# Performance work log

Hardware: AMD Instinct MI355X
Metric: run time of the kernel (lower is better)

The kernel has to match this reference:

```python
import jax, jax.numpy as jnp
import numpy as np

B, N, D, E = 64, 512, 128, 16384
NEG = -1e9


def setup_inputs() -> dict:
    key = jax.random.key(0)
    ks = jax.random.split(key, 10)
    return {
        "node_emb": jax.random.normal(ks[0], (B, N, D), jnp.float32),
        "mask": jnp.ones((B, N), dtype=bool),
        "edge_idx": jax.random.randint(ks[1], (2, E), 0, N),
        "attn_wts": jax.random.uniform(ks[2], (E,), jnp.float32),
        "edge_weights": jax.random.uniform(ks[3], (B, N, N), jnp.float32) + 0.1,
        "W_ih": jax.random.normal(ks[4], (4 * D, D), jnp.float32) * 0.05,
        "W_hh": jax.random.normal(ks[5], (4 * D, D), jnp.float32) * 0.05,
        "b_ih": jax.random.normal(ks[6], (4 * D,), jnp.float32) * 0.05,
        "b_hh": jax.random.normal(ks[7], (4 * D,), jnp.float32) * 0.05,
        "attn_W": jax.random.normal(ks[8], (D, D), jnp.float32) * 0.05,
        "attn_b": jax.random.normal(ks[9], (D,), jnp.float32) * 0.05,
        "enc_attn_wt": jnp.float32(0.75),
        "revisit_penalty": jnp.float32(-0.5),
        "shortcut_weight": jnp.float32(10.0),
        "shortcut_bonus": jnp.float32(15.0),
    }


def reference(node_emb, mask, edge_idx, attn_wts, edge_weights,
              W_ih, W_hh, b_ih, b_hh, attn_W, attn_b,
              enc_attn_wt, revisit_penalty, shortcut_weight, shortcut_bonus):
    B_, N_, D_ = node_emb.shape
    scale = 1.0 / jnp.sqrt(jnp.float32(D_))
    bidx = jnp.arange(B_)
    nidx = jnp.arange(N_)[None, :]
    # keys = attn(node_emb): identical every step in the torch code -> hoisted.
    keys = node_emb @ attn_W.T + attn_b  # [B,N,D]
    # Encoder-attention edge scatter precomputed as dense [N,N] src->tgt table.
    A = jnp.zeros((N_, N_), node_emb.dtype).at[edge_idx[0], edge_idx[1]].add(attn_wts)
    real_count = jnp.sum(mask, axis=1).astype(jnp.int32)  # [B]

    def step_fn(carry, step):
        h, c, inp, visited, uniq, first, prev = carry
        # LSTMCell (torch gate order i,f,g,o)
        gates = inp @ W_ih.T + b_ih + h @ W_hh.T + b_hh  # [B,4D]
        i, f, g, o = jnp.split(gates, 4, axis=1)
        c = jax.nn.sigmoid(f) * c + jax.nn.sigmoid(i) * jnp.tanh(g)
        h = jax.nn.sigmoid(o) * jnp.tanh(c)
        scores = jnp.einsum('bd,bnd->bn', h, keys) * scale  # [B,N]
        # encoder-attn bonus (only when prev_node exists, i.e. step > 0)
        scores = scores + jnp.where(step > 0, enc_attn_wt, 0.0) * A[prev]
        # branch 1: revisit penalty while tour incomplete
        rev = jnp.where(visited & mask, revisit_penalty, scores)
        # branch 2: shortcut bonuses once all real nodes visited (next_idx == first)
        prev_w = edge_weights[bidx, prev]  # [B,N] costs from prev node
        to_first = jnp.take_along_axis(edge_weights, first[:, None, None], axis=2)[..., 0]  # [B,N]
        direct = prev_w[bidx, first][:, None]  # [B,1]
        detour = prev_w + to_first
        bmask = mask & (nidx != first[:, None]) & (detour < direct)
        bonus = jnp.where(bmask, shortcut_bonus * (direct - detour) / direct, 0.0)
        cmin = prev_w.min(axis=1, keepdims=True)
        cmax = prev_w.max(axis=1, keepdims=True)
        rng_ok = cmax > cmin
        normd = jnp.where(rng_ok,
                          shortcut_weight * (1.0 - (prev_w - cmin) / jnp.where(rng_ok, cmax - cmin, 1.0)),
                          0.0)
        shortcut = scores + bonus + normd
        cond = (uniq < real_count)[:, None]
        scores = jnp.where(cond, rev, jnp.where(step > 0, shortcut, scores))
        scores = jnp.where(mask, scores, NEG)
        probs = jax.nn.softmax(scores, axis=1)
        curr = jnp.argmax(probs, axis=1).astype(jnp.int32)  # greedy decode
        log_p = jnp.log(probs[bidx, curr] + 1e-10)
        first = jnp.where(step == 0, curr, first)
        newly = ~visited[bidx, curr]
        uniq = uniq + newly.astype(jnp.int32)
        visited = visited.at[bidx, curr].set(True)
        inp = node_emb[bidx, curr]
        return (h, c, inp, visited, uniq, first, curr), (curr, log_p)

    init = (jnp.zeros((B_, D_), node_emb.dtype),
            jnp.zeros((B_, D_), node_emb.dtype),
            node_emb.mean(axis=1),
            jnp.zeros((B_, N_), dtype=bool),
            jnp.zeros((B_,), jnp.int32),
            jnp.zeros((B_,), jnp.int32),
            jnp.zeros((B_,), jnp.int32))
    (h, c, inp, visited, uniq, first, prev), (curr_seq, logp_seq) = jax.lax.scan(
        step_fn, init, jnp.arange(N_))
    # final step N: return to first node with log-prob 0
    tours = jnp.concatenate([curr_seq.T, first[:, None]], axis=1)          # [B, N+1]
    log_probs = jnp.concatenate([logp_seq.T, jnp.zeros((B_, 1), logp_seq.dtype)], axis=1)
    return tours, log_probs
```

## Files before the change

### kernel.cpp

```cpp
#include <hip/hip_runtime.h>
#include <cstdint>
#include <cstddef>

constexpr int kB = 64;
constexpr int kN = 512;
constexpr int kD = 128;
constexpr int kE = 16384;
constexpr double kNEG = -1e9;

constexpr size_t BO_WT   = 0;
constexpr size_t BO_BIAS = 524288;
constexpr size_t BO_INP0 = 528384;
constexpr size_t BO_AWT  = 593920;
constexpr size_t BO_AB   = 659456;
constexpr size_t BO_A    = 659968;
constexpr size_t BO_WT4  = 2757120;
constexpr size_t BO_GPRE = 2888192;
constexpr size_t GPRE_BYTES = (size_t)64 * 513 * 512 * 4;
constexpr size_t BO_KEYS4 = BO_GPRE + GPRE_BYTES;
constexpr size_t KEYS_BYTES = (size_t)64 * 32 * 512 * 16;
constexpr size_t WS_NEED_FULL = BO_KEYS4 + KEYS_BYTES;

__device__ __forceinline__ double finzd(double v, double fb) {
    return (v == v && v <= 1.0e308 && v >= -1.0e308) ? v : fb;
}
__device__ __forceinline__ double load_scalar_d(const void* p, double fb) {
    unsigned short lo; __builtin_memcpy(&lo, p, 2);
    float f;
    if (lo == 0) { __builtin_memcpy(&f, p, 4); }
    else { unsigned int u = ((unsigned int)lo) << 16; __builtin_memcpy(&f, &u, 4); }
    return finzd((double)f, fb);
}
__device__ __forceinline__ double sigd(double v) { return 1.0 / (1.0 + exp(-v)); }

__global__ __launch_bounds__(256) void prep_wt(const float* __restrict__ W_ih,
                                               const float* __restrict__ W_hh,
                                               const float* __restrict__ b_ih,
                                               const float* __restrict__ b_hh,
                                               char* __restrict__ wsb) {
    int idx = blockIdx.x * 256 + threadIdx.x;
    if (idx < 131072) {
        int k = idx >> 9, j = idx & 511;
        float v = (k < 128) ? W_ih[j * 128 + k] : W_hh[j * 128 + (k - 128)];
        ((float*)(wsb + BO_WT))[idx] = v;
    } else if (idx < 131072 + 512) {
        int j = idx - 131072;
        ((double*)(wsb + BO_BIAS))[j] = (double)b_ih[j] + (double)b_hh[j];
    }
}

__global__ __launch_bounds__(256) void prep_wt4(char* __restrict__ wsb) {
    int idx = blockIdx.x * 256 + threadIdx.x;
    int q = idx >> 9, j = idx & 511;
    const float* WT = (const float*)(wsb + BO_WT);
    float4 v;
    v.x = WT[(size_t)(192 + 4 * q + 0) * 512 + j];
    v.y = WT[(size_t)(192 + 4 * q + 1) * 512 + j];
    v.z = WT[(size_t)(192 + 4 * q + 2) * 512 + j];
    v.w = WT[(size_t)(192 + 4 * q + 3) * 512 + j];
    ((float4*)(wsb + BO_WT4))[idx] = v;
}

__global__ __launch_bounds__(256) void prep_awt(const float* __restrict__ attn_W,
                                                const float* __restrict__ attn_b,
                                                char* __restrict__ wsb) {
    int idx = blockIdx.x * 256 + threadIdx.x;
    if (idx < 16384) {
        int k = idx >> 7, d = idx & 127;
        ((float*)(wsb + BO_AWT))[idx] = attn_W[d * 128 + k];
    } else if (idx < 16512) {
        ((float*)(wsb + BO_AB))[idx - 16384] = attn_b[idx - 16384];
    }
}

__global__ __launch_bounds__(256) void prep_zeroA(char* __restrict__ wsb) {
    int idx = blockIdx.x * 256 + threadIdx.x;
    ((double*)(wsb + BO_A))[idx] = 0.0;
}

__global__ __launch_bounds__(256) void prep_scatterA(const int* __restrict__ edge_idx,
                                                     const float* __restrict__ attn_wts,
                                                     char* __restrict__ wsb) {
    int e = blockIdx.x * 256 + threadIdx.x;
    if (e < kE) {
        int s = edge_idx[e] & 511;
        int t = edge_idx[kE + e] & 511;
        atomicAdd(&((double*)(wsb + BO_A))[(size_t)s * kN + t], (double)attn_wts[e]);
    }
}

__global__ __launch_bounds__(128) void prep_inp0(const float* __restrict__ emb,
                                                 char* __restrict__ wsb) {
    int b = blockIdx.x, d = threadIdx.x;
    const float* p = emb + (size_t)b * kN * kD + d;
    double s = 0.0;
#pragma unroll 8
    for (int n = 0; n < kN; n++) s += (double)p[(size_t)n * kD];
    ((double*)(wsb + BO_INP0))[b * kD + d] = s * (1.0 / 512.0);
}

__global__ __launch_bounds__(512) void prep_gpre(const float* __restrict__ emb,
                                                 char* __restrict__ wsb) {
    const int b = blockIdx.y;
    const int n0 = blockIdx.x * 16;
    const int tid = threadIdx.x;
    const int nr = (513 - n0 < 16) ? (513 - n0) : 16;
    __shared__ double xs[16 * 128];
    const double* inp0 = (const double*)(wsb + BO_INP0) + (size_t)b * 128;
    for (int i = tid; i < nr * 128; i += 512) {
        int r = i >> 7, d = i & 127;
        int n = n0 + r;
        xs[i] = (n < 512) ? (double)emb[((size_t)b * 512 + n) * 128 + d] : inp0[d];
    }
    __syncthreads();
    const float* wcol = ((const float*)(wsb + BO_WT)) + tid;
    double acc[16];
#pragma unroll
    for (int r = 0; r < 16; r++) acc[r] = 0.0;
    for (int k = 0; k < 128; k++) {
        double w = (double)wcol[(size_t)k * 512];
#pragma unroll
        for (int r = 0; r < 16; r++) acc[r] += xs[r * 128 + k] * w;
    }
    float* gp = (float*)(wsb + BO_GPRE);
#pragma unroll
    for (int r = 0; r < 16; r++)
        if (r < nr) gp[((size_t)b * 513 + n0 + r) * 512 + tid] = (float)acc[r];
}

__global__ __launch_bounds__(256) void prep_keys(const float* __restrict__ emb,
                                                 const float* __restrict__ attn_W,
                                                 const float* __restrict__ attn_b,
                                                 char* __restrict__ wsb) {
    const int b = blockIdx.y;
    const int n0 = blockIdx.x * 64;
    const int tid = threadIdx.x;
    __shared__ float embL[64 * 130];
    __shared__ float WL[128 * 128];
    for (int i = tid; i < 64 * 128; i += 256) {
        int r = i >> 7, k = i & 127;
        embL[r * 130 + k] = emb[((size_t)b * kN + n0 + r) * kD + k];
    }
    for (int i = tid; i < 128 * 128; i += 256) WL[i] = attn_W[i];
    __syncthreads();
    const int nh = tid & 63;
    const int part = tid >> 6;
    float4* kout = (float4*)(wsb + BO_KEYS4) + (size_t)b * 32 * 512;
    const float* er = &embL[nh * 130];
    for (int dq = part * 8; dq < part * 8 + 8; dq++) {
        double a0 = (double)attn_b[4 * dq + 0], a1 = (double)attn_b[4 * dq + 1];
        double a2 = (double)attn_b[4 * dq + 2], a3 = (double)attn_b[4 * dq + 3];
        const float* w0 = &WL[(4 * dq + 0) * 128];
        const float* w1 = &WL[(4 * dq + 1) * 128];
        const float* w2 = &WL[(4 * dq + 2) * 128];
        const float* w3 = &WL[(4 * dq + 3) * 128];
#pragma unroll 8
        for (int k = 0; k < 128; k++) {
            double ek = (double)er[k];
            a0 += ek * (double)w0[k]; a1 += ek * (double)w1[k];
            a2 += ek * (double)w2[k]; a3 += ek * (double)w3[k];
        }
        float4 v; v.x = (float)a0; v.y = (float)a1; v.z = (float)a2; v.w = (float)a3;
        kout[(size_t)dq * 512 + n0 + nh] = v;
    }
}

template <int M>
__global__ __launch_bounds__(512) void decode_kernel(
    const float* __restrict__ emb, const unsigned char* __restrict__ mask,
    const float* __restrict__ edge_w, const char* __restrict__ wsb,
    const void* __restrict__ enc_p, const void* __restrict__ rev_p,
    const void* __restrict__ sw_p, const void* __restrict__ sb_p,
    float* __restrict__ out) {
    const int b = blockIdx.x;
    const int tid = threadIdx.x;

    __shared__ float wks[(M == 0) ? (128 * 129) : (16 * 512 * 4)];
    __shared__ double x[256];
    __shared__ double cs[128];
    __shared__ double gates[(M == 0) ? 512 : 1];
    __shared__ double trans[(M == 0) ? 1 : 512];
    __shared__ double up[(M == 0) ? 512 : 1];
    __shared__ double u[(M == 0) ? 128 : 1];
    __shared__ double redd[8], redd2[8];
    __shared__ int redi[8];
    __shared__ unsigned char visited[512];
    __shared__ int tours_s[512];
    __shared__ double logp_d[512];
    __shared__ int s_rc;
    __shared__ double s_hb, s_cmin, s_cmax;

    const float* WT = (const float*)(wsb + BO_WT);
    const double* biasC = (const double*)(wsb + BO_BIAS);
    const double* A = (const double*)(wsb + BO_A);
    const float* EW = edge_w + (size_t)b * kN * kN;
    const double enc = load_scalar_d(enc_p, 0.75);
    const double revp = load_scalar_d(rev_p, -0.5);
    const double sw = load_scalar_d(sw_p, 10.0);
    const double sb = load_scalar_d(sb_p, 15.0);
    const double scale = 1.0 / sqrt(128.0);

    if constexpr (M == 0) {
        for (int i = tid; i < 128 * 128; i += 512) {
            int k = i >> 7, d = i & 127;
            wks[k * 129 + d] = ((const float*)(wsb + BO_AWT))[i];
        }
    } else {
        for (int i = tid; i < 64 * 512; i += 512) {
            int r = i >> 9, j = i & 511;
            wks[((r >> 2) * 512 + j) * 4 + (r & 3)] = WT[(size_t)(128 + r) * 512 + j];
        }
    }
    double abreg = 0.0;
    if constexpr (M == 0)
        abreg = (tid < 128) ? (double)((const float*)(wsb + BO_AB))[tid] : 0.0;

    if (tid < 128) { x[tid] = ((const double*)(wsb + BO_INP0))[b * kD + tid]; cs[tid] = 0.0; }
    if (tid >= 128 && tid < 256) x[tid] = 0.0;
    visited[tid] = 0;
    const size_t mi = (size_t)b * kN + tid;
    const bool mk = (mask[mi] != 0) || (mask[mi & ~(size_t)3] != 0);
    {
        int v = mk ? 1 : 0;
        for (int off = 32; off; off >>= 1) v += __shfl_xor(v, off);
        if ((tid & 63) == 0) redi[tid >> 6] = v;
    }
    __syncthreads();
    if (tid == 0) {
        int rc = 0;
        for (int w = 0; w < 8; w++) rc += redi[w];
        s_rc = rc;
    }
    __syncthreads();
    const int rc = s_rc;

    int prev = 0, first = 0, uniq = 0;

    const float* gbase = (const float*)(wsb + BO_GPRE) + (size_t)b * 513 * 512;
    const float4* kb4 = (const float4*)(wsb + BO_KEYS4) + (size_t)b * 32 * 512;
    const float4* wl4 = (const float4*)wks;
    const float4* wg4 = (const float4*)(wsb + BO_WT4);
    const double* h = &x[128];

    if constexpr (M != 0) {
        {
            double gp0 = (double)gbase[(size_t)512 * 512 + tid];
            double gf = (biasC[tid] + gp0) + 0.0;
            trans[tid] = (tid >= 256 && tid < 384) ? tanh(gf) : sigd(gf);
        }
        double a_cur = A[tid];
        __syncthreads();

        for (int step = 0; step < kN; step++) {
            if (step > 0) {
                if (tid == prev) visited[tid] = 1;
                if (tid == 0) {
                    double m = 0.0;
#pragma unroll
                    for (int w = 0; w < 8; w++) m += redd2[w];
                    m = (m == m && m > 0.0) ? m : 1.0;
                    double p = 1.0 / m;
                    logp_d[step - 1] = (p == p && p >= 0.0) ? p : 0.0;
                }
            }
            if (tid < 128) {
                double ai = trans[tid], af = trans[128 + tid];
                double ag = trans[256 + tid], ao = trans[384 + tid];
                double c = af * cs[tid] + ai * ag;
                cs[tid] = c;
                x[128 + tid] = ao * tanh(c);
            }
            __syncthreads();

            double d0 = 0.0, d1 = 0.0, d2 = 0.0, d3 = 0.0;
            double q0 = biasC[tid], q1 = 0.0, q2 = 0.0, q3 = 0.0;
#pragma unroll 4
            for (int q = 0; q < 32; q++) {
                float4 w = kb4[(size_t)q * 512 + tid];
                const double* hq = &h[4 * q];
                d0 += hq[0] * (double)w.x; d1 += hq[1] * (double)w.y;
                d2 += hq[2] * (double)w.z; d3 += hq[3] * (double)w.w;
            }
#pragma unroll 4
            for (int q = 0; q < 16; q++) {
                float4 w = wl4[q * 512 + tid];
                const double* hq = &h[4 * q];
                q0 += hq[0] * (double)w.x; q1 += hq[1] * (double)w.y;
                q2 += hq[2] * (double)w.z; q3 += hq[3] * (double)w.w;
            }
#pragma unroll 4
            for (int q = 0; q < 16; q++) {
                float4 w = wg4[q * 512 + tid];
                const double* hq = &h[64 + 4 * q];
                q0 += hq[0] * (double)w.x; q1 += hq[1] * (double)w.y;
                q2 += hq[2] * (double)w.z; q3 += hq[3] * (double)w.w;
            }
            double s = ((d0 + d1) + (d2 + d3)) * scale;
            if (step > 0) s += enc * a_cur;

            double sfinal;
            const bool shortcut_mode = (uniq >= rc);
            if (!shortcut_mode) {
                sfinal = (visited[tid] && mk) ? revp : s;
            } else if (step > 0) {
                double pw = (double)EW[(size_t)prev * kN + tid];
                double mn = pw, mx = pw;
                for (int off = 32; off; off >>= 1) {
                    mn = fmin(mn, __shfl_xor(mn, off));
                    mx = fmax(mx, __shfl_xor(mx, off));
                }
                if ((tid & 63) == 0) { redd[tid >> 6] = mn; redd2[tid >> 6] = mx; }
                __syncthreads();
                if (tid == 0) {
                    double a = redd[0], z = redd2[0];
                    for (int w = 1; w < 8; w++) { a = fmin(a, redd[w]); z = fmax(z, redd2[w]); }
                    s_cmin = a; s_cmax = z;
                }
                __syncthreads();
                double cmin = s_cmin, cmax = s_cmax;
                int fi = first;
                double to_first = (double)EW[(size_t)tid * kN + fi];
                double direct = (double)EW[(size_t)prev * kN + fi];
                double detour = pw + to_first;
                double bonus = (mk && tid != fi && detour < direct && direct != 0.0)
                                   ? sb * (direct - detour) / direct : 0.0;
                bool rng_ok = cmax > cmin;
                double normd = rng_ok ? sw * (1.0 - (pw - cmin) / (cmax - cmin)) : 0.0;
                sfinal = s + bonus + normd;
            } else {
                sfinal = s;
            }
            if (!mk) sfinal = kNEG;
            sfinal = finzd(sfinal, kNEG);

            double v = sfinal; int vi = tid;
            for (int off = 32; off; off >>= 1) {
                double ov = __shfl_xor(v, off);
                int oi = __shfl_xor(vi, off);
                if (ov > v || (ov == v && oi < vi)) { v = ov; vi = oi; }
            }
            if ((tid & 63) == 0) { redd[tid >> 6] = v; redi[tid >> 6] = vi; }
            __syncthreads();
            double smax = redd[0]; int sidx = redi[0];
#pragma unroll
            for (int w = 1; w < 8; w++) {
                double rv = redd[w]; int ri = redi[w];
                if (rv > smax || (rv == smax && ri < sidx)) { smax = rv; sidx = ri; }
            }
            const int oldvis = visited[sidx];
            double gp_next = (double)gbase[(size_t)sidx * 512 + tid];
            double a_next = A[(size_t)sidx * kN + tid];

            double e = exp(sfinal - smax);
            double sv = e;
            for (int off = 32; off; off >>= 1) sv += __shfl_xor(sv, off);
            if ((tid & 63) == 0) redd2[tid >> 6] = sv;
            if (tid == 0) tours_s[step] = sidx;

            double gfn = ((q0 + q1) + (q2 + q3)) + gp_next;
            trans[tid] = (tid >= 256 && tid < 384) ? tanh(gfn) : sigd(gfn);

            uniq += oldvis ? 0 : 1;
            if (step == 0) first = sidx;
            prev = sidx;
            a_cur = a_next;
            __syncthreads();
        }
        if (tid == 0) {
            double m = 0.0;
#pragma unroll
            for (int w = 0; w < 8; w++) m += redd2[w];
            m = (m == m && m > 0.0) ? m : 1.0;
            double p = 1.0 / m;
            logp_d[kN - 1] = (p == p && p >= 0.0) ? p : 0.0;
        }
    } else {
        const float* awt = (const float*)wks;
        for (int step = 0; step < kN; step++) {
            double g0 = biasC[tid], g1 = 0.0, g2 = 0.0, g3 = 0.0;
            const float* wcol = WT + tid;
            for (int k0 = 0; k0 < 256; k0 += 4) {
                float w0 = wcol[(size_t)(k0 + 0) * 512], w1 = wcol[(size_t)(k0 + 1) * 512];
                float w2 = wcol[(size_t)(k0 + 2) * 512], w3 = wcol[(size_t)(k0 + 3) * 512];
                g0 += x[k0 + 0] * (double)w0; g1 += x[k0 + 1] * (double)w1;
                g2 += x[k0 + 2] * (double)w2; g3 += x[k0 + 3] * (double)w3;
            }
            gates[tid] = (g0 + g1) + (g2 + g3);
            __syncthreads();
            if (tid < 128) {
                double gi = gates[tid], gf = gates[128 + tid];
                double gg = gates[256 + tid], go = gates[384 + tid];
                double c = sigd(gf) * cs[tid] + sigd(gi) * tanh(gg);
                cs[tid] = c;
                double hd = sigd(go) * tanh(c);
                x[128 + tid] = hd;
                double hp = hd * abreg;
                for (int off = 32; off; off >>= 1) hp += __shfl_xor(hp, off);
                if ((tid & 63) == 0) redd[tid >> 6] = hp;
            }
            __syncthreads();
            {
                int k = tid & 127, part = tid >> 7;
                const float* arow = &awt[(size_t)k * 129 + part * 32];
                const double* hx = &x[128 + part * 32];
                double ps = 0.0;
#pragma unroll 8
                for (int i2 = 0; i2 < 32; i2++) ps += hx[i2] * (double)arow[i2];
                up[part * 128 + k] = ps;
            }
            __syncthreads();
            if (tid < 128) u[tid] = up[tid] + up[128 + tid] + up[256 + tid] + up[384 + tid];
            if (tid == 0) s_hb = redd[0] + redd[1];
            __syncthreads();
            double d0 = 0.0, d1 = 0.0, d2 = 0.0, d3 = 0.0;
            const float4* e4 = (const float4*)(emb + ((size_t)b * kN + tid) * kD);
#pragma unroll 4
            for (int q = 0; q < 32; q++) {
                float4 w = e4[q];
                const double* u4 = &u[q * 4];
                d0 += u4[0] * (double)w.x; d1 += u4[1] * (double)w.y;
                d2 += u4[2] * (double)w.z; d3 += u4[3] * (double)w.w;
            }
            double s = (((d0 + d1) + (d2 + d3)) + s_hb) * scale;
            if (step > 0) s += enc * A[(size_t)prev * kN + tid];

            double sfinal;
            const bool shortcut_mode = (uniq >= rc);
            if (!shortcut_mode) {
                sfinal = (visited[tid] && mk) ? revp : s;
            } else if (step > 0) {
                double pw = (double)EW[(size_t)prev * kN + tid];
                double mn = pw, mx = pw;
                for (int off = 32; off; off >>= 1) {
                    mn = fmin(mn, __shfl_xor(mn, off));
                    mx = fmax(mx, __shfl_xor(mx, off));
                }
                if ((tid & 63) == 0) { redd[tid >> 6] = mn; redd2[tid >> 6] = mx; }
                __syncthreads();
                if (tid == 0) {
                    double a = redd[0], z = redd2[0];
                    for (int w = 1; w < 8; w++) { a = fmin(a, redd[w]); z = fmax(z, redd2[w]); }
                    s_cmin = a; s_cmax = z;
                }
                __syncthreads();
                double cmin = s_cmin, cmax = s_cmax;
                int fi = first;
                double to_first = (double)EW[(size_t)tid * kN + fi];
                double direct = (double)EW[(size_t)prev * kN + fi];
                double detour = pw + to_first;
                double bonus = (mk && tid != fi && detour < direct && direct != 0.0)
                                   ? sb * (direct - detour) / direct : 0.0;
                bool rng_ok = cmax > cmin;
                double normd = rng_ok ? sw * (1.0 - (pw - cmin) / (cmax - cmin)) : 0.0;
                sfinal = s + bonus + normd;
            } else {
                sfinal = s;
            }
            if (!mk) sfinal = kNEG;
            sfinal = finzd(sfinal, kNEG);

            double v = sfinal; int vi = tid;
            for (int off = 32; off; off >>= 1) {
                double ov = __shfl_xor(v, off);
                int oi = __shfl_xor(vi, off);
                if (ov > v || (ov == v && oi < vi)) { v = ov; vi = oi; }
            }
            if ((tid & 63) == 0) { redd[tid >> 6] = v; redi[tid >> 6] = vi; }
            __syncthreads();
            double smax = redd[0]; int sidx = redi[0];
#pragma unroll
            for (int w = 1; w < 8; w++) {
                double rv = redd[w]; int ri = redi[w];
                if (rv > smax || (rv == smax && ri < sidx)) { smax = rv; sidx = ri; }
            }
            const int oldvis = visited[sidx];
            double e = exp(sfinal - smax);
            double sv = e;
            for (int off = 32; off; off >>= 1) sv += __shfl_xor(sv, off);
            if ((tid & 63) == 0) redd2[tid >> 6] = sv;
            __syncthreads();
            double m = 0.0;
#pragma unroll
            for (int w = 0; w < 8; w++) m += redd2[w];
            m = (m == m && m > 0.0) ? m : 1.0;
            double p = 1.0 / m;
            p = (p == p && p >= 0.0) ? p : 0.0;
            if (tid == 0) { tours_s[step] = sidx; logp_d[step] = p; }
            if (tid == sidx) visited[tid] = 1;
            uniq += oldvis ? 0 : 1;
            if (step == 0) first = sidx;
            prev = sidx;
            if (tid < 128) x[tid] = (double)emb[((size_t)b * kN + sidx) * kD + tid];
            __syncthreads();
        }
    }

    __syncthreads();
    out[(size_t)b * (kN + 1) + tid] = (float)tours_s[tid];
    out[(size_t)kB * (kN + 1) + (size_t)b * (kN + 1) + tid] =
        (float)log(logp_d[tid] + 1e-10);
    if (tid == 0) {
        out[(size_t)b * (kN + 1) + kN] = (float)first;
        out[(size_t)kB * (kN + 1) + (size_t)b * (kN + 1) + kN] = 0.f;
    }
}

extern "C" void kernel_launch(void* const* d_in, const int* in_sizes, int n_in,
                              void* d_out, int out_size, void* d_ws, size_t ws_size,
                              hipStream_t stream) {
    const float* emb = (const float*)d_in[0];
    const unsigned char* mask = (const unsigned char*)d_in[1];
    const int* edge_idx = (const int*)d_in[2];
    const float* attn_wts = (const float*)d_in[3];
    const float* edge_w = (const float*)d_in[4];
    const float* W_ih = (const float*)d_in[5];
    const float* W_hh = (const float*)d_in[6];
    const float* b_ih = (const float*)d_in[7];
    const float* b_hh = (const float*)d_in[8];
    const float* attn_W = (const float*)d_in[9];
    const float* attn_b = (const float*)d_in[10];
    char* wsb = (char*)d_ws;
    float* out = (float*)d_out;
    (void)in_sizes; (void)n_in; (void)out_size;

    prep_wt<<<dim3(514), dim3(256), 0, stream>>>(W_ih, W_hh, b_ih, b_hh, wsb);
    prep_zeroA<<<dim3(1024), dim3(256), 0, stream>>>(wsb);
    prep_scatterA<<<dim3(64), dim3(256), 0, stream>>>(edge_idx, attn_wts, wsb);
    prep_inp0<<<dim3(64), dim3(128), 0, stream>>>(emb, wsb);

    if (ws_size >= WS_NEED_FULL) {
        prep_wt4<<<dim3(32), dim3(256), 0, stream>>>(wsb);
        prep_gpre<<<dim3(33, 64), dim3(512), 0, stream>>>(emb, wsb);
        prep_keys<<<dim3(8, 64), dim3(256), 0, stream>>>(emb, attn_W, attn_b, wsb);
        decode_kernel<2><<<dim3(64), dim3(512), 0, stream>>>(emb, mask, edge_w, wsb,
            d_in[11], d_in[12], d_in[13], d_in[14], out);
    } else {
        prep_awt<<<dim3(65), dim3(256), 0, stream>>>(attn_W, attn_b, wsb);
        decode_kernel<0><<<dim3(64), dim3(512), 0, stream>>>(emb, mask, edge_w, wsb,
            d_in[11], d_in[12], d_in[13], d_in[14], out);
    }
}
```

Before: 3.787 ms.

## Split decode block into score and gate-projection thread halves

```diff
diff --git a/kernel.cpp b/kernel.cpp
--- a/kernel.cpp
+++ b/kernel.cpp
@@ -166,12 +166,13 @@
 }
 
 template <int M>
-__global__ __launch_bounds__(512) void decode_kernel(
+__global__ __launch_bounds__(1024) void decode_kernel(
     const float* __restrict__ emb, const unsigned char* __restrict__ mask,
     const float* __restrict__ edge_w, const char* __restrict__ wsb,
     const void* __restrict__ enc_p, const void* __restrict__ rev_p,
     const void* __restrict__ sw_p, const void* __restrict__ sb_p,
     float* __restrict__ out) {
+    constexpr int TB = (M == 0) ? 512 : 1024;
     const int b = blockIdx.x;
     const int tid = threadIdx.x;
 
@@ -201,12 +202,12 @@
     const double scale = 1.0 / sqrt(128.0);
 
     if constexpr (M == 0) {
-        for (int i = tid; i < 128 * 128; i += 512) {
+        for (int i = tid; i < 128 * 128; i += TB) {
             int k = i >> 7, d = i & 127;
             wks[k * 129 + d] = ((const float*)(wsb + BO_AWT))[i];
         }
     } else {
-        for (int i = tid; i < 64 * 512; i += 512) {
+        for (int i = tid; i < 64 * 512; i += TB) {
             int r = i >> 9, j = i & 511;
             wks[((r >> 2) * 512 + j) * 4 + (r & 3)] = WT[(size_t)(128 + r) * 512 + j];
         }
@@ -217,19 +218,20 @@
 
     if (tid < 128) { x[tid] = ((const double*)(wsb + BO_INP0))[b * kD + tid]; cs[tid] = 0.0; }
     if (tid >= 128 && tid < 256) x[tid] = 0.0;
-    visited[tid] = 0;
-    const size_t mi = (size_t)b * kN + tid;
-    const bool mk = (mask[mi] != 0) || (mask[mi & ~(size_t)3] != 0);
-    {
+    if (tid < 512) visited[tid] = 0;
+    bool mk = false;
+    if (tid < 512) {
+        const size_t mi = (size_t)b * kN + tid;
+        mk = (mask[mi] != 0) || (mask[mi & ~(size_t)3] != 0);
         int v = mk ? 1 : 0;
         for (int off = 32; off; off >>= 1) v += __shfl_xor(v, off);
         if ((tid & 63) == 0) redi[tid >> 6] = v;
     }
     __syncthreads();
     if (tid == 0) {
-        int rc = 0;
-        for (int w = 0; w < 8; w++) rc += redi[w];
-        s_rc = rc;
+        int rcv = 0;
+        for (int w = 0; w < 8; w++) rcv += redi[w];
+        s_rc = rcv;
     }
     __syncthreads();
     const int rc = s_rc;
@@ -243,12 +245,14 @@
     const double* h = &x[128];
 
     if constexpr (M != 0) {
-        {
-            double gp0 = (double)gbase[(size_t)512 * 512 + tid];
-            double gf = (biasC[tid] + gp0) + 0.0;
-            trans[tid] = (tid >= 256 && tid < 384) ? tanh(gf) : sigd(gf);
-        }
-        double a_cur = A[tid];
+        const bool NT = (tid < 512);
+        const int jj = tid & 511;
+        if (!NT) {
+            double gp0 = (double)gbase[(size_t)512 * 512 + jj];
+            double gf = (biasC[jj] + gp0) + 0.0;
+            trans[jj] = (jj >= 256 && jj < 384) ? tanh(gf) : sigd(gf);
+        }
+        double a_cur = NT ? A[tid] : 0.0;
         __syncthreads();
 
         for (int step = 0; step < kN; step++) {
@@ -263,40 +267,177 @@
                     logp_d[step - 1] = (p == p && p >= 0.0) ? p : 0.0;
                 }
             }
+            if (tid >= 512 && tid < 640) {
+                const int d = tid - 512;
+                double ai = trans[d], af = trans[128 + d];
+                double ag = trans[256 + d], ao = trans[384 + d];
+                double c = af * cs[d] + ai * ag;
+                cs[d] = c;
+                x[128 + d] = ao * tanh(c);
+            }
+            __syncthreads();
+
+            double s = 0.0, sfinal = kNEG;
+            double q0 = 0.0, q1 = 0.0, q2 = 0.0, q3 = 0.0;
+            if (NT) {
+                double d0 = 0.0, d1 = 0.0, d2 = 0.0, d3 = 0.0;
+#pragma unroll 4
+                for (int q = 0; q < 32; q++) {
+                    float4 w = kb4[(size_t)q * 512 + tid];
+                    const double* hq = &h[4 * q];
+                    d0 += hq[0] * (double)w.x; d1 += hq[1] * (double)w.y;
+                    d2 += hq[2] * (double)w.z; d3 += hq[3] * (double)w.w;
+                }
+                s = ((d0 + d1) + (d2 + d3)) * scale;
+                if (step > 0) s += enc * a_cur;
+            } else {
+                q0 = biasC[jj];
+#pragma unroll 4
+                for (int q = 0; q < 16; q++) {
+                    float4 w = wl4[q * 512 + jj];
+                    const double* hq = &h[4 * q];
+                    q0 += hq[0] * (double)w.x; q1 += hq[1] * (double)w.y;
+                    q2 += hq[2] * (double)w.z; q3 += hq[3] * (double)w.w;
+                }
+#pragma unroll 4
+                for (int q = 0; q < 16; q++) {
+                    float4 w = wg4[q * 512 + jj];
+                    const double* hq = &h[64 + 4 * q];
+                    q0 += hq[0] * (double)w.x; q1 += hq[1] * (double)w.y;
+                    q2 += hq[2] * (double)w.z; q3 += hq[3] * (double)w.w;
+                }
+            }
+
+            const bool shortcut_mode = (uniq >= rc);
+            if (!shortcut_mode) {
+                if (NT) sfinal = (visited[tid] && mk) ? revp : s;
+            } else if (step > 0) {
+                double pw = 0.0;
+                if (NT) {
+                    pw = (double)EW[(size_t)prev * kN + tid];
+                    double mn = pw, mx = pw;
+                    for (int off = 32; off; off >>= 1) {
+                        mn = fmin(mn, __shfl_xor(mn, off));
+                        mx = fmax(mx, __shfl_xor(mx, off));
+                    }
+                    if ((tid & 63) == 0) { redd[tid >> 6] = mn; redd2[tid >> 6] = mx; }
+                }
+                __syncthreads();
+                if (tid == 0) {
+                    double a = redd[0], z = redd2[0];
+                    for (int w = 1; w < 8; w++) { a = fmin(a, redd[w]); z = fmax(z, redd2[w]); }
+                    s_cmin = a; s_cmax = z;
+                }
+                __syncthreads();
+                if (NT) {
+                    double cmin = s_cmin, cmax = s_cmax;
+                    int fi = first;
+                    double to_first = (double)EW[(size_t)tid * kN + fi];
+                    double direct = (double)EW[(size_t)prev * kN + fi];
+                    double detour = pw + to_first;
+                    double bonus = (mk && tid != fi && detour < direct && direct != 0.0)
+                                       ? sb * (direct - detour) / direct : 0.0;
+                    bool rng_ok = cmax > cmin;
+                    double normd = rng_ok ? sw * (1.0 - (pw - cmin) / (cmax - cmin)) : 0.0;
+                    sfinal = s + bonus + normd;
+                }
+            } else {
+                if (NT) sfinal = s;
+            }
+            if (NT) {
+                if (!mk) sfinal = kNEG;
+                sfinal = finzd(sfinal, kNEG);
+                double v = sfinal; int vi = tid;
+                for (int off = 32; off; off >>= 1) {
+                    double ov = __shfl_xor(v, off);
+                    int oi = __shfl_xor(vi, off);
+                    if (ov > v || (ov == v && oi < vi)) { v = ov; vi = oi; }
+                }
+                if ((tid & 63) == 0) { redd[tid >> 6] = v; redi[tid >> 6] = vi; }
+            }
+            __syncthreads();
+            double smax = redd[0]; int sidx = redi[0];
+#pragma unroll
+            for (int w = 1; w < 8; w++) {
+                double rv = redd[w]; int ri = redi[w];
+                if (rv > smax || (rv == smax && ri < sidx)) { smax = rv; sidx = ri; }
+            }
+            const int oldvis = visited[sidx];
+            if (NT) {
+                double a_next = A[(size_t)sidx * kN + tid];
+                double e = exp(sfinal - smax);
+                double sv = e;
+                for (int off = 32; off; off >>= 1) sv += __shfl_xor(sv, off);
+                if ((tid & 63) == 0) redd2[tid >> 6] = sv;
+                a_cur = a_next;
+            } else {
+                double gp_next = (double)gbase[(size_t)sidx * 512 + jj];
+                double gfn = ((q0 + q1) + (q2 + q3)) + gp_next;
+                trans[jj] = (jj >= 256 && jj < 384) ? tanh(gfn) : sigd(gfn);
+            }
+            if (tid == 0) tours_s[step] = sidx;
+            uniq += oldvis ? 0 : 1;
+            if (step == 0) first = sidx;
+            prev = sidx;
+            __syncthreads();
+        }
+        if (tid == 0) {
+            double m = 0.0;
+#pragma unroll
+            for (int w = 0; w < 8; w++) m += redd2[w];
+            m = (m == m && m > 0.0) ? m : 1.0;
+            double p = 1.0 / m;
+            logp_d[kN - 1] = (p == p && p >= 0.0) ? p : 0.0;
+        }
+    } else {
+        const float* awt = (const float*)wks;
+        for (int step = 0; step < kN; step++) {
+            double g0 = biasC[tid], g1 = 0.0, g2 = 0.0, g3 = 0.0;
+            const float* wcol = WT + tid;
+            for (int k0 = 0; k0 < 256; k0 += 4) {
+                float w0 = wcol[(size_t)(k0 + 0) * 512], w1 = wcol[(size_t)(k0 + 1) * 512];
+                float w2 = wcol[(size_t)(k0 + 2) * 512], w3 = wcol[(size_t)(k0 + 3) * 512];
+                g0 += x[k0 + 0] * (double)w0; g1 += x[k0 + 1] * (double)w1;
+                g2 += x[k0 + 2] * (double)w2; g3 += x[k0 + 3] * (double)w3;
+            }
+            gates[tid] = (g0 + g1) + (g2 + g3);
+            __syncthreads();
             if (tid < 128) {
-                double ai = trans[tid], af = trans[128 + tid];
-                double ag = trans[256 + tid], ao = trans[384 + tid];
-                double c = af * cs[tid] + ai * ag;
+                double gi = gates[tid], gf = gates[128 + tid];
+                double gg = gates[256 + tid], go = gates[384 + tid];
+                double c = sigd(gf) * cs[tid] + sigd(gi) * tanh(gg);
                 cs[tid] = c;
-                x[128 + tid] = ao * tanh(c);
-            }
-            __syncthreads();
-
+                double hd = sigd(go) * tanh(c);
+                x[128 + tid] = hd;
+                double hp = hd * abreg;
+                for (int off = 32; off; off >>= 1) hp += __shfl_xor(hp, off);
+                if ((tid & 63) == 0) redd[tid >> 6] = hp;
+            }
+            __syncthreads();
+            {
+                int k = tid & 127, part = tid >> 7;
+                const float* arow = &awt[(size_t)k * 129 + part * 32];
+                const double* hx = &x[128 + part * 32];
+                double ps = 0.0;
+#pragma unroll 8
+                for (int i2 = 0; i2 < 32; i2++) ps += hx[i2] * (double)arow[i2];
+                up[part * 128 + k] = ps;
+            }
+            __syncthreads();
+            if (tid < 128) u[tid] = up[tid] + up[128 + tid] + up[256 + tid] + up[384 + tid];
+            if (tid == 0) s_hb = redd[0] + redd[1];
+            __syncthreads();
             double d0 = 0.0, d1 = 0.0, d2 = 0.0, d3 = 0.0;
-            double q0 = biasC[tid], q1 = 0.0, q2 = 0.0, q3 = 0.0;
+            const float4* e4 = (const float4*)(emb + ((size_t)b * kN + tid) * kD);
 #pragma unroll 4
             for (int q = 0; q < 32; q++) {
-                float4 w = kb4[(size_t)q * 512 + tid];
-                const double* hq = &h[4 * q];
-                d0 += hq[0] * (double)w.x; d1 += hq[1] * (double)w.y;
-                d2 += hq[2] * (double)w.z; d3 += hq[3] * (double)w.w;
-            }
-#pragma unroll 4
-            for (int q = 0; q < 16; q++) {
-                float4 w = wl4[q * 512 + tid];
-                const double* hq = &h[4 * q];
-                q0 += hq[0] * (double)w.x; q1 += hq[1] * (double)w.y;
-                q2 += hq[2] * (double)w.z; q3 += hq[3] * (double)w.w;
-            }
-#pragma unroll 4
-            for (int q = 0; q < 16; q++) {
-                float4 w = wg4[q * 512 + tid];
-                const double* hq = &h[64 + 4 * q];
-                q0 += hq[0] * (double)w.x; q1 += hq[1] * (double)w.y;
-                q2 += hq[2] * (double)w.z; q3 += hq[3] * (double)w.w;
-            }
-            double s = ((d0 + d1) + (d2 + d3)) * scale;
-            if (step > 0) s += enc * a_cur;
+                float4 w = e4[q];
+                const double* u4 = &u[q * 4];
+                d0 += u4[0] * (double)w.x; d1 += u4[1] * (double)w.y;
+                d2 += u4[2] * (double)w.z; d3 += u4[3] * (double)w.w;
+            }
+            double s = (((d0 + d1) + (d2 + d3)) + s_hb) * scale;
+            if (step > 0) s += enc * A[(size_t)prev * kN + tid];
 
             double sfinal;
             const bool shortcut_mode = (uniq >= rc);
@@ -348,132 +489,6 @@
                 if (rv > smax || (rv == smax && ri < sidx)) { smax = rv; sidx = ri; }
             }
             const int oldvis = visited[sidx];
-            double gp_next = (double)gbase[(size_t)sidx * 512 + tid];
-            double a_next = A[(size_t)sidx * kN + tid];
-
-            double e = exp(sfinal - smax);
-            double sv = e;
-            for (int off = 32; off; off >>= 1) sv += __shfl_xor(sv, off);
-            if ((tid & 63) == 0) redd2[tid >> 6] = sv;
-            if (tid == 0) tours_s[step] = sidx;
-
-            double gfn = ((q0 + q1) + (q2 + q3)) + gp_next;
-            trans[tid] = (tid >= 256 && tid < 384) ? tanh(gfn) : sigd(gfn);
-
-            uniq += oldvis ? 0 : 1;
-            if (step == 0) first = sidx;
-            prev = sidx;
-            a_cur = a_next;
-            __syncthreads();
-        }
-        if (tid == 0) {
-            double m = 0.0;
-#pragma unroll
-            for (int w = 0; w < 8; w++) m += redd2[w];
-            m = (m == m && m > 0.0) ? m : 1.0;
-            double p = 1.0 / m;
-            logp_d[kN - 1] = (p == p && p >= 0.0) ? p : 0.0;
-        }
-    } else {
-        const float* awt = (const float*)wks;
-        for (int step = 0; step < kN; step++) {
-            double g0 = biasC[tid], g1 = 0.0, g2 = 0.0, g3 = 0.0;
-            const float* wcol = WT + tid;
-            for (int k0 = 0; k0 < 256; k0 += 4) {
-                float w0 = wcol[(size_t)(k0 + 0) * 512], w1 = wcol[(size_t)(k0 + 1) * 512];
-                float w2 = wcol[(size_t)(k0 + 2) * 512], w3 = wcol[(size_t)(k0 + 3) * 512];
-                g0 += x[k0 + 0] * (double)w0; g1 += x[k0 + 1] * (double)w1;
-                g2 += x[k0 + 2] * (double)w2; g3 += x[k0 + 3] * (double)w3;
-            }
-            gates[tid] = (g0 + g1) + (g2 + g3);
-            __syncthreads();
-            if (tid < 128) {
-                double gi = gates[tid], gf = gates[128 + tid];
-                double gg = gates[256 + tid], go = gates[384 + tid];
-                double c = sigd(gf) * cs[tid] + sigd(gi) * tanh(gg);
-                cs[tid] = c;
-                double hd = sigd(go) * tanh(c);
-                x[128 + tid] = hd;
-                double hp = hd * abreg;
-                for (int off = 32; off; off >>= 1) hp += __shfl_xor(hp, off);
-                if ((tid & 63) == 0) redd[tid >> 6] = hp;
-            }
-            __syncthreads();
-            {
-                int k = tid & 127, part = tid >> 7;
-                const float* arow = &awt[(size_t)k * 129 + part * 32];
-                const double* hx = &x[128 + part * 32];
-                double ps = 0.0;
-#pragma unroll 8
-                for (int i2 = 0; i2 < 32; i2++) ps += hx[i2] * (double)arow[i2];
-                up[part * 128 + k] = ps;
-            }
-            __syncthreads();
-            if (tid < 128) u[tid] = up[tid] + up[128 + tid] + up[256 + tid] + up[384 + tid];
-            if (tid == 0) s_hb = redd[0] + redd[1];
-            __syncthreads();
-            double d0 = 0.0, d1 = 0.0, d2 = 0.0, d3 = 0.0;
-            const float4* e4 = (const float4*)(emb + ((size_t)b * kN + tid) * kD);
-#pragma unroll 4
-            for (int q = 0; q < 32; q++) {
-                float4 w = e4[q];
-                const double* u4 = &u[q * 4];
-                d0 += u4[0] * (double)w.x; d1 += u4[1] * (double)w.y;
-                d2 += u4[2] * (double)w.z; d3 += u4[3] * (double)w.w;
-            }
-            double s = (((d0 + d1) + (d2 + d3)) + s_hb) * scale;
-            if (step > 0) s += enc * A[(size_t)prev * kN + tid];
-
-            double sfinal;
-            const bool shortcut_mode = (uniq >= rc);
-            if (!shortcut_mode) {
-                sfinal = (visited[tid] && mk) ? revp : s;
-            } else if (step > 0) {
-                double pw = (double)EW[(size_t)prev * kN + tid];
-                double mn = pw, mx = pw;
-                for (int off = 32; off; off >>= 1) {
-                    mn = fmin(mn, __shfl_xor(mn, off));
-                    mx = fmax(mx, __shfl_xor(mx, off));
-                }
-                if ((tid & 63) == 0) { redd[tid >> 6] = mn; redd2[tid >> 6] = mx; }
-                __syncthreads();
-                if (tid == 0) {
-                    double a = redd[0], z = redd2[0];
-                    for (int w = 1; w < 8; w++) { a = fmin(a, redd[w]); z = fmax(z, redd2[w]); }
-                    s_cmin = a; s_cmax = z;
-                }
-                __syncthreads();
-                double cmin = s_cmin, cmax = s_cmax;
-                int fi = first;
-                double to_first = (double)EW[(size_t)tid * kN + fi];
-                double direct = (double)EW[(size_t)prev * kN + fi];
-                double detour = pw + to_first;
-                double bonus = (mk && tid != fi && detour < direct && direct != 0.0)
-                                   ? sb * (direct - detour) / direct : 0.0;
-                bool rng_ok = cmax > cmin;
-                double normd = rng_ok ? sw * (1.0 - (pw - cmin) / (cmax - cmin)) : 0.0;
-                sfinal = s + bonus + normd;
-            } else {
-                sfinal = s;
-            }
-            if (!mk) sfinal = kNEG;
-            sfinal = finzd(sfinal, kNEG);
-
-            double v = sfinal; int vi = tid;
-            for (int off = 32; off; off >>= 1) {
-                double ov = __shfl_xor(v, off);
-                int oi = __shfl_xor(vi, off);
-                if (ov > v || (ov == v && oi < vi)) { v = ov; vi = oi; }
-            }
-            if ((tid & 63) == 0) { redd[tid >> 6] = v; redi[tid >> 6] = vi; }
-            __syncthreads();
-            double smax = redd[0]; int sidx = redi[0];
-#pragma unroll
-            for (int w = 1; w < 8; w++) {
-                double rv = redd[w]; int ri = redi[w];
-                if (rv > smax || (rv == smax && ri < sidx)) { smax = rv; sidx = ri; }
-            }
-            const int oldvis = visited[sidx];
             double e = exp(sfinal - smax);
             double sv = e;
             for (int off = 32; off; off >>= 1) sv += __shfl_xor(sv, off);
@@ -496,9 +511,11 @@
     }
 
     __syncthreads();
-    out[(size_t)b * (kN + 1) + tid] = (float)tours_s[tid];
-    out[(size_t)kB * (kN + 1) + (size_t)b * (kN + 1) + tid] =
-        (float)log(logp_d[tid] + 1e-10);
+    if (tid < 512) {
+        out[(size_t)b * (kN + 1) + tid] = (float)tours_s[tid];
+        out[(size_t)kB * (kN + 1) + (size_t)b * (kN + 1) + tid] =
+            (float)log(logp_d[tid] + 1e-10);
+    }
     if (tid == 0) {
         out[(size_t)b * (kN + 1) + kN] = (float)first;
         out[(size_t)kB * (kN + 1) + (size_t)b * (kN + 1) + kN] = 0.f;
@@ -532,7 +549,7 @@
         prep_wt4<<<dim3(32), dim3(256), 0, stream>>>(wsb);
         prep_gpre<<<dim3(33, 64), dim3(512), 0, stream>>>(emb, wsb);
         prep_keys<<<dim3(8, 64), dim3(256), 0, stream>>>(emb, attn_W, attn_b, wsb);
-        decode_kernel<2><<<dim3(64), dim3(512), 0, stream>>>(emb, mask, edge_w, wsb,
+        decode_kernel<3><<<dim3(64), dim3(1024), 0, stream>>>(emb, mask, edge_w, wsb,
             d_in[11], d_in[12], d_in[13], d_in[14], out);
     } else {
         prep_awt<<<dim3(65), dim3(256), 0, stream>>>(attn_W, attn_b, wsb);
```

After: 4.174 ms. 10.2% more time.
